# Kernel tuning notes

Hardware: AMD Instinct MI355X
Metric: run time of the kernel (lower is better)

Reference implementation:

```python
import math
import jax, jax.numpy as jnp
import numpy as np

N_HEADS, INPUT_DIM, EMBED_DIM = 8, 512, 512
KEY_DIM = EMBED_DIM // N_HEADS  # 64, val_dim == key_dim
BATCH, N = 4, 2048


def setup_inputs() -> dict:
    key = jax.random.key(0)
    ks = jax.random.split(key, 6)
    def unif(k, shape):
        stdv = 1.0 / math.sqrt(shape[-1])
        return jax.random.uniform(k, shape, jnp.float32, -stdv, stdv)
    q = jax.random.normal(ks[0], (BATCH, N, INPUT_DIM), jnp.float32)
    mask = jax.random.randint(ks[1], (BATCH, N, N), 0, 2, jnp.int32)
    W_query = unif(ks[2], (N_HEADS, INPUT_DIM, KEY_DIM))
    W_key = unif(ks[3], (N_HEADS, INPUT_DIM, KEY_DIM))
    W_val = unif(ks[4], (N_HEADS, INPUT_DIM, KEY_DIM))
    W_out = unif(ks[5], (N_HEADS, KEY_DIM, EMBED_DIM))
    return {"q": q, "mask": mask, "W_query": W_query, "W_key": W_key,
            "W_val": W_val, "W_out": W_out}


def reference(q, mask, W_query, W_key, W_val, W_out):
    # Self-attention: k is None, v is None -> k = q, v = q (module forward_).
    norm = 1.0 / math.sqrt(KEY_DIM)
    m = mask.astype(bool)[None]  # (1, b, nq, ng) broadcast over heads
    Q = jnp.einsum('bnd,hdk->hbnk', q, W_query)  # (h, b, nq, dk)
    K = jnp.einsum('bnd,hdk->hbnk', q, W_key)    # (h, b, ng, dk)
    V = jnp.einsum('bnd,hdv->hbnv', q, W_val)    # (h, b, ng, dv)
    scores = norm * jnp.einsum('hbqk,hbgk->hbqg', Q, K)  # (h, b, nq, ng)
    scores = jnp.where(m, -jnp.inf, scores)
    attn = jax.nn.softmax(scores, axis=-1)
    attn = jnp.where(m, 0.0, attn)  # zero out masked (also kills NaN rows)
    heads = jnp.einsum('hbqg,hbgv->hbqv', attn, V)
    out = jnp.einsum('hbqv,hve->bqe', heads, W_out)  # (b, nq, embed)
    return out
```

## Files before the change

kernel.cpp:

```cpp
#include <hip/hip_runtime.h>
#include <hip/hip_bf16.h>
#include <stdint.h>

using bf16 = __hip_bfloat16;
typedef __attribute__((ext_vector_type(8))) short short8;
typedef __attribute__((ext_vector_type(4))) short short4b;
typedef __attribute__((ext_vector_type(4))) float f32x4;
typedef __attribute__((ext_vector_type(4))) unsigned int u32x4;

#if __has_builtin(__builtin_amdgcn_exp2f)
#define EXP2(x) __builtin_amdgcn_exp2f(x)
#else
#define EXP2(x) exp2f(x)
#endif

__device__ __forceinline__ short8 load8(const bf16* p) {
  return *reinterpret_cast<const short8*>(p);
}
__device__ __forceinline__ short f2b(float f) {
  return __builtin_bit_cast(short, __float2bfloat16(f));
}
__device__ __forceinline__ unsigned int pk2(float a, float b) {
  return (unsigned int)(unsigned short)f2b(a) |
         ((unsigned int)(unsigned short)f2b(b) << 16);
}
__device__ __forceinline__ void asy16(const bf16* g, bf16* l) {
  __builtin_amdgcn_global_load_lds(
      (const __attribute__((address_space(1))) void*)g,
      (__attribute__((address_space(3))) void*)l, 16, 0, 0);
}


__global__ void k_prep(const float4* __restrict__ x, ushort4* __restrict__ xb,
                       const float* __restrict__ Wq, const float* __restrict__ Wk,
                       const float* __restrict__ Wv, const float* __restrict__ Wo,
                       bf16* __restrict__ Wcat, bf16* __restrict__ Wot,
                       const int4* __restrict__ m4,
                       unsigned long long* __restrict__ bits) {
  int blk = blockIdx.x;
  const int tid = threadIdx.x;
  if (blk < 4096) {
    int i = blk * 256 + tid;
    float4 v = x[i];
    ushort4 o;
    o.x = (unsigned short)f2b(v.x);
    o.y = (unsigned short)f2b(v.y);
    o.z = (unsigned short)f2b(v.z);
    o.w = (unsigned short)f2b(v.w);
    xb[i] = o;
  } else if (blk < 4352) {
    int t = blk - 4096;
    __shared__ float T[64][65];
    if (t < 192) {
      int which = t >> 6;
      int h = (t >> 3) & 7, dt = t & 7;
      const float* W = (which == 0) ? Wq : ((which == 1) ? Wk : Wv);
#pragma unroll
      for (int p = 0; p < 4; ++p) {
        int row = p * 16 + (tid >> 4);
        float4 v = *(const float4*)(W + (size_t)(h * 512 + dt * 64 + row) * 64 +
                                    (tid & 15) * 4);
        T[row][(tid & 15) * 4 + 0] = v.x;
        T[row][(tid & 15) * 4 + 1] = v.y;
        T[row][(tid & 15) * 4 + 2] = v.z;
        T[row][(tid & 15) * 4 + 3] = v.w;
      }
      __syncthreads();
      float scale = (which == 0) ? 0.18033688011112042f : 1.0f;
      int jj = tid >> 2, i0 = (tid & 3) * 16;
#pragma unroll
      for (int q = 0; q < 2; ++q) {
        short8 o;
#pragma unroll
        for (int e = 0; e < 8; ++e) o[e] = f2b(T[i0 + q * 8 + e][jj] * scale);
        *(short8*)(Wcat + (size_t)(which * 512 + h * 64 + jj) * 512 + dt * 64 +
                   i0 + q * 8) = o;
      }
    } else {
      int t2 = t - 192;
      int h = t2 >> 3, et = t2 & 7;
#pragma unroll
      for (int p = 0; p < 4; ++p) {
        int row = p * 16 + (tid >> 4);
        float4 v = *(const float4*)(Wo + (size_t)(h * 64 + row) * 512 + et * 64 +
                                    (tid & 15) * 4);
        T[row][(tid & 15) * 4 + 0] = v.x;
        T[row][(tid & 15) * 4 + 1] = v.y;
        T[row][(tid & 15) * 4 + 2] = v.z;
        T[row][(tid & 15) * 4 + 3] = v.w;
      }
      __syncthreads();
      int jj = tid >> 2, i0 = (tid & 3) * 16;
#pragma unroll
      for (int q = 0; q < 2; ++q) {
        short8 o;
#pragma unroll
        for (int e = 0; e < 8; ++e) o[e] = f2b(T[i0 + q * 8 + e][jj]);
        *(short8*)(Wot + (size_t)(et * 64 + jj) * 512 + h * 64 + i0 + q * 8) = o;
      }
    }
  } else {
    int i = (blk - 4352) * 256 + tid;
    int4 v = m4[i];
    unsigned int nib = (unsigned)(v.x != 0) | ((unsigned)(v.y != 0) << 1) |
                       ((unsigned)(v.z != 0) << 2) | ((unsigned)(v.w != 0) << 3);
    unsigned long long w = (unsigned long long)nib << (4 * (tid & 15));
    w |= __shfl_xor(w, 1);
    w |= __shfl_xor(w, 2);
    w |= __shfl_xor(w, 4);
    w |= __shfl_xor(w, 8);
    if ((tid & 15) == 0) bits[i >> 4] = w;
  }
}

__device__ __forceinline__ void gemm128(const bf16* __restrict__ A,
                                        const bf16* __restrict__ Bt,
                                        bf16* As, bf16* Bs,
                                        int rowBase, int colBase,
                                        f32x4 acc[4][4]) {
  const int tid = threadIdx.x;
  const int lane = tid & 63, w = tid >> 6;
  const int g = lane >> 4, r = lane & 15;

  auto stage = [&](int buf, int s) {
#pragma unroll
    for (int p = 0; p < 2; ++p) {
      int c = p * 256 + tid;
      int row = c >> 2, gr = c & 3, sg = gr ^ (row & 3);
      asy16(A + (size_t)(rowBase + row) * 512 + s * 32 + sg * 8,
            As + buf * 4096 + c * 8);
    }
#pragma unroll
    for (int p = 0; p < 2; ++p) {
      int c = p * 256 + tid;
      int row = c >> 2, gr = c & 3, sg = gr ^ (row & 3);
      asy16(Bt + (size_t)(colBase + row) * 512 + s * 32 + sg * 8,
            Bs + buf * 4096 + c * 8);
    }
  };

  stage(0, 0);
  int buf = 0;
  const int rbl = (w >> 1) * 64, cbl = (w & 1) * 64;
  for (int s = 0; s < 16; ++s) {
    __syncthreads();
    if (s < 15) stage(buf ^ 1, s + 1);
    const bf16* a0 = As + buf * 4096;
    const bf16* b0 = Bs + buf * 4096;
    short8 af[4], bfr[4];
#pragma unroll
    for (int mt = 0; mt < 4; ++mt) {
      int row = rbl + mt * 16 + r;
      af[mt] = load8(a0 + (row * 4 + (g ^ (row & 3))) * 8);
    }
#pragma unroll
    for (int nt = 0; nt < 4; ++nt) {
      int col = cbl + nt * 16 + r;
      bfr[nt] = load8(b0 + (col * 4 + (g ^ (col & 3))) * 8);
    }
#pragma unroll
    for (int mt = 0; mt < 4; ++mt)
#pragma unroll
      for (int nt = 0; nt < 4; ++nt)
        acc[mt][nt] = __builtin_amdgcn_mfma_f32_16x16x32_bf16(
            af[mt], bfr[nt], acc[mt][nt], 0, 0, 0);
    buf ^= 1;
  }
}

__global__ __launch_bounds__(256, 3) void k_proj_qkv(
    const bf16* __restrict__ Xb, const bf16* __restrict__ Wcat,
    bf16* __restrict__ Qb, bf16* __restrict__ Kp, bf16* __restrict__ Vp) {
  __shared__ __align__(16) bf16 As[2 * 4096];
  __shared__ __align__(16) bf16 Bs[2 * 4096];
  int rowBase = blockIdx.x * 128, colBase = blockIdx.y * 128;
  f32x4 acc[4][4] = {};
  gemm128(Xb, Wcat, As, Bs, rowBase, colBase, acc);
  const int lane = threadIdx.x & 63, w = threadIdx.x >> 6;
  const int g = lane >> 4, r = lane & 15;
#pragma unroll
  for (int mt = 0; mt < 4; ++mt) {
    int row0 = rowBase + (w >> 1) * 64 + mt * 16 + 4 * g;
    int b = row0 >> 11, n0 = row0 & 2047;
    int kt = n0 >> 6;
#pragma unroll
    for (int nt = 0; nt < 4; ++nt) {
      int col = colBase + (w & 1) * 64 + nt * 16 + r;
      if (col < 512) {
        int hh = col >> 6, dk = col & 63;
        bf16* p0 = Qb + ((size_t)(b * 8 + hh) * 2048 + n0) * 64 + dk;
#pragma unroll
        for (int rr = 0; rr < 4; ++rr)
          p0[rr * 64] = __float2bfloat16(acc[mt][nt][rr]);
      } else if (col < 1024) {
        int hh = (col >> 6) & 7, dk = col & 63;
        int half = dk >> 5, gk = (dk >> 3) & 3, jj = dk & 7;
        int kr = n0 & 63;
        int kc = kr >> 4, r0 = kr & 15;
        bf16* base = Kp + (size_t)(b * 8 + hh) * 131072 + (size_t)kt * 4096 +
                     ((kc * 2 + half) * 4 + gk) * 128 + jj;
#pragma unroll
        for (int rr = 0; rr < 4; ++rr)
          base[(r0 + rr) * 8] = __float2bfloat16(acc[mt][nt][rr]);
      } else {
        int hdv = col - 1024;
        int hh = hdv >> 6, dv = hdv & 63;
        int dvs = dv >> 4, rv = dv & 15;
        int kcol0 = n0 & 63;
        int half = kcol0 >> 5, gv = (kcol0 >> 2) & 3;
        int j0 = ((kcol0 >> 4) & 1) * 4;
        short4b pkv;
#pragma unroll
        for (int rr = 0; rr < 4; ++rr) pkv[rr] = f2b(acc[mt][nt][rr]);
        *reinterpret_cast<short4b*>(
            Vp + (size_t)(b * 8 + hh) * 131072 + (size_t)kt * 4096 +
            (((half * 4 + dvs) * 4 + gv) * 16 + rv) * 8 + j0) = pkv;
      }
    }
  }
}

__global__ __launch_bounds__(256, 2) void k_proj_out(
    const bf16* __restrict__ O, const bf16* __restrict__ Wot,
    float* __restrict__ out) {
  __shared__ __align__(16) bf16 As[2 * 4096];
  __shared__ __align__(16) bf16 Bs[2 * 4096];
  int rowBase = blockIdx.x * 128, colBase = blockIdx.y * 128;
  f32x4 acc[4][4] = {};
  gemm128(O, Wot, As, Bs, rowBase, colBase, acc);
  const int lane = threadIdx.x & 63, w = threadIdx.x >> 6;
  const int g = lane >> 4, r = lane & 15;
#pragma unroll
  for (int mt = 0; mt < 4; ++mt) {
    int row0 = rowBase + (w >> 1) * 64 + mt * 16 + 4 * g;
#pragma unroll
    for (int nt = 0; nt < 4; ++nt) {
      int col = colBase + (w & 1) * 64 + nt * 16 + r;
#pragma unroll
      for (int rr = 0; rr < 4; ++rr)
        out[(size_t)(row0 + rr) * 512 + col] = acc[mt][nt][rr];
    }
  }
}

__global__ __launch_bounds__(256, 4) void k_attn(const bf16* __restrict__ Q,
    const bf16* __restrict__ K, const bf16* __restrict__ V,
    const unsigned long long* __restrict__ MB, bf16* __restrict__ O) {
  const int blin = blockIdx.x;
  const int j = blin >> 3;
  const int bh = (blin & 7) * 4 + (j >> 5);
  const int qt = j & 31;
  const int b = bh >> 3, h = bh & 7;
  const int tid = threadIdx.x;
  const int lane = tid & 63;
  const int wave = tid >> 6;
  const int g = lane >> 4, r = lane & 15;
  const int qbase = qt * 64 + wave * 16;

  __shared__ __align__(16) bf16 Kl[2][4096];
  __shared__ __align__(16) bf16 Vl[2][4096];

  const bf16* Kp = K + (size_t)bh * 131072;
  const bf16* Vp = V + (size_t)bh * 131072;

  short8 qf0, qf1;
  {
    const bf16* Qp = Q + ((size_t)bh * 2048 + qbase + r) * 64;
    qf0 = load8(Qp + g * 8);
    qf1 = load8(Qp + 32 + g * 8);
  }
  const unsigned long long* Mp = MB + ((size_t)b * 2048 + qbase + r) * 32;

  short8 ones;
#pragma unroll
  for (int i = 0; i < 8; ++i) ones[i] = (short)0x3F80;

  f32x4 acc[4] = {};
  f32x4 acc_l = {};

  auto stageK = [&](int buf, int kt) {
    const bf16* Kg = Kp + (size_t)kt * 4096;
    asy16(Kg + tid * 8, &Kl[buf][0] + tid * 8);
    asy16(Kg + 2048 + tid * 8, &Kl[buf][0] + 2048 + tid * 8);
  };
  auto stageV = [&](int buf, int kt) {
    const bf16* Vg = Vp + (size_t)kt * 4096;
    asy16(Vg + tid * 8, &Vl[buf][0] + tid * 8);
    asy16(Vg + 2048 + tid * 8, &Vl[buf][0] + 2048 + tid * 8);
  };

  auto qk = [&](const bf16* kl, f32x4 stl[4]) {
#pragma unroll
    for (int kc = 0; kc < 4; ++kc) {
      short8 kf0 = load8(kl + ((kc * 2 + 0) * 4 + g) * 128 + r * 8);
      short8 kf1 = load8(kl + ((kc * 2 + 1) * 4 + g) * 128 + r * 8);
      f32x4 z = {};
      z = __builtin_amdgcn_mfma_f32_16x16x32_bf16(kf0, qf0, z, 0, 0, 0);
      stl[kc] = __builtin_amdgcn_mfma_f32_16x16x32_bf16(kf1, qf1, z, 0, 0, 0);
    }
  };

  stageK(0, 0);
  stageK(1, 1);
  stageV(0, 0);
  unsigned long long mw0, mw1;
  mw0 = Mp[0];
  __syncthreads();
  f32x4 st0[4], st1[4];
  qk(&Kl[0][0], st0);

#define ATTN_ITER(KT, CUR, NXT, SC, SN, MC, MN)                              \
  do {                                                                       \
    __syncthreads();                                                         \
    if ((KT) < 30) stageK(CUR, (KT) + 2);                                    \
    if ((KT) < 31) {                                                         \
      stageV(NXT, (KT) + 1);                                                 \
      MN = Mp[(KT) + 1];                                                     \
    }                                                                        \
    __builtin_amdgcn_s_setprio(1);                                           \
    if ((KT) < 31) qk(&Kl[NXT][0], SN);                                      \
    __builtin_amdgcn_s_setprio(0);                                           \
    unsigned ml = (unsigned)MC >> (4 * g);                                   \
    unsigned mh = (unsigned)(MC >> 32) >> (4 * g);                           \
    float p[16];                                                             \
    _Pragma("unroll") for (int kc = 0; kc < 4; ++kc)                         \
        _Pragma("unroll") for (int rr = 0; rr < 4; ++rr) {                   \
      float e = EXP2(SC[kc][rr]);                                            \
      unsigned wsel = (kc & 2) ? mh : ml;                                    \
      bool bad = (wsel >> (((kc & 1) << 4) + rr)) & 1u;                      \
      p[kc * 4 + rr] = bad ? 0.f : e;                                        \
    }                                                                        \
    u32x4 q0, q1;                                                            \
    _Pragma("unroll") for (int i2 = 0; i2 < 4; ++i2) {                       \
      q0[i2] = pk2(p[2 * i2], p[2 * i2 + 1]);                                \
      q1[i2] = pk2(p[8 + 2 * i2], p[8 + 2 * i2 + 1]);                        \
    }                                                                        \
    short8 pa0 = __builtin_bit_cast(short8, q0);                             \
    short8 pa1 = __builtin_bit_cast(short8, q1);                             \
    acc_l = __builtin_amdgcn_mfma_f32_16x16x32_bf16(pa0, ones, acc_l, 0, 0, 0); \
    acc_l = __builtin_amdgcn_mfma_f32_16x16x32_bf16(pa1, ones, acc_l, 0, 0, 0); \
    const bf16* vl = &Vl[CUR][0];                                            \
    __builtin_amdgcn_s_setprio(1);                                           \
    _Pragma("unroll") for (int dvs = 0; dvs < 4; ++dvs) {                    \
      short8 vb0 = load8(vl + ((0 * 4 + dvs) * 4 + g) * 128 + r * 8);        \
      short8 vb1 = load8(vl + ((1 * 4 + dvs) * 4 + g) * 128 + r * 8);        \
      acc[dvs] = __builtin_amdgcn_mfma_f32_16x16x32_bf16(pa0, vb0, acc[dvs], 0, 0, 0); \
      acc[dvs] = __builtin_amdgcn_mfma_f32_16x16x32_bf16(pa1, vb1, acc[dvs], 0, 0, 0); \
    }                                                                        \
    __builtin_amdgcn_s_setprio(0);                                           \
  } while (0)

  for (int t = 0; t < 16; ++t) {
    const int kt = 2 * t;
    ATTN_ITER(kt, 0, 1, st0, st1, mw0, mw1);
    ATTN_ITER(kt + 1, 1, 0, st1, st0, mw1, mw0);
  }
#undef ATTN_ITER

  float inv[4];
#pragma unroll
  for (int rr = 0; rr < 4; ++rr)
    inv[rr] = (acc_l[rr] > 0.f) ? 1.f / acc_l[rr] : 0.f;
  bf16* Op = O + ((size_t)b * 2048 + qbase + 4 * g) * 512 + h * 64;
#pragma unroll
  for (int dvs = 0; dvs < 4; ++dvs)
#pragma unroll
    for (int rr = 0; rr < 4; ++rr)
      Op[rr * 512 + dvs * 16 + r] = __float2bfloat16(acc[dvs][rr] * inv[rr]);
}


extern "C" void kernel_launch(void* const* d_in, const int* in_sizes, int n_in,
                              void* d_out, int out_size, void* d_ws, size_t ws_size,
                              hipStream_t stream) {
  const float* q    = (const float*)d_in[0];
  const int*   mask = (const int*)d_in[1];
  const float* Wq   = (const float*)d_in[2];
  const float* Wk   = (const float*)d_in[3];
  const float* Wv   = (const float*)d_in[4];
  const float* Wo   = (const float*)d_in[5];
  float* out = (float*)d_out;

  char* ws = (char*)d_ws;
  const size_t MB1 = 1024 * 1024;
  bf16* Xb   = (bf16*)(ws + 0);
  bf16* Qb   = (bf16*)(ws + 8 * MB1);
  bf16* Kpm  = (bf16*)(ws + 16 * MB1);
  bf16* Vpm  = (bf16*)(ws + 24 * MB1);
  bf16* Ob   = (bf16*)(ws + 32 * MB1);
  unsigned long long* Mbits = (unsigned long long*)(ws + 40 * MB1);
  bf16* Wcat = (bf16*)(ws + 42 * MB1);
  bf16* Wot  = (bf16*)(ws + 42 * MB1 + 1536 * 512 * 2);

  k_prep<<<20736, 256, 0, stream>>>((const float4*)q, (ushort4*)Xb,
                                    Wq, Wk, Wv, Wo, Wcat, Wot,
                                    (const int4*)mask, Mbits);
  k_proj_qkv<<<dim3(64, 12), 256, 0, stream>>>(Xb, Wcat, Qb, Kpm, Vpm);
  k_attn<<<1024, 256, 0, stream>>>(Qb, Kpm, Vpm, Mbits, Ob);
  k_proj_out<<<dim3(64, 4), 256, 0, stream>>>(Ob, Wot, out);
}
```

Before: 207.2 us.

## Double attention block size with triple-buffered K/V and smaller out-proj tiles

The attention kernel now runs 512-thread blocks covering 128 queries, so each staged K/V tile is shared by twice as many waves. K and V staging moves to a three-buffer ring, loaded together two tiles ahead, with one asynchronous copy per thread per tile. The output projection switches to 64x128 tiles with a new GEMM helper, doubling its block count to fill the GPU better. The O buffer now aliases the Xb workspace region, which relies on Xb no longer being needed after the QKV projection; the larger blocks and bigger shared-memory footprint may lower attention occupancy.

Measured after the change: 205.2 us. No clear change (-1.0%).

```diff
diff --git a/kernel.cpp b/kernel.cpp
--- a/kernel.cpp
+++ b/kernel.cpp
@@ -168,6 +168,60 @@
   }
 }
 
+__device__ __forceinline__ void gemm64x128(const bf16* __restrict__ A,
+                                           const bf16* __restrict__ Bt,
+                                           bf16* As, bf16* Bs,
+                                           int rowBase, int colBase,
+                                           f32x4 acc[2][4]) {
+  const int tid = threadIdx.x;
+  const int lane = tid & 63, w = tid >> 6;
+  const int g = lane >> 4, r = lane & 15;
+
+  auto stage = [&](int buf, int s) {
+    {
+      int c = tid;
+      int row = c >> 2, gr = c & 3, sg = gr ^ (row & 3);
+      asy16(A + (size_t)(rowBase + row) * 512 + s * 32 + sg * 8,
+            As + buf * 2048 + c * 8);
+    }
+#pragma unroll
+    for (int p = 0; p < 2; ++p) {
+      int c = p * 256 + tid;
+      int row = c >> 2, gr = c & 3, sg = gr ^ (row & 3);
+      asy16(Bt + (size_t)(colBase + row) * 512 + s * 32 + sg * 8,
+            Bs + buf * 4096 + c * 8);
+    }
+  };
+
+  stage(0, 0);
+  int buf = 0;
+  const int rbl = (w >> 1) * 32, cbl = (w & 1) * 64;
+  for (int s = 0; s < 16; ++s) {
+    __syncthreads();
+    if (s < 15) stage(buf ^ 1, s + 1);
+    const bf16* a0 = As + buf * 2048;
+    const bf16* b0 = Bs + buf * 4096;
+    short8 af[2], bfr[4];
+#pragma unroll
+    for (int mt = 0; mt < 2; ++mt) {
+      int row = rbl + mt * 16 + r;
+      af[mt] = load8(a0 + (row * 4 + (g ^ (row & 3))) * 8);
+    }
+#pragma unroll
+    for (int nt = 0; nt < 4; ++nt) {
+      int col = cbl + nt * 16 + r;
+      bfr[nt] = load8(b0 + (col * 4 + (g ^ (col & 3))) * 8);
+    }
+#pragma unroll
+    for (int mt = 0; mt < 2; ++mt)
+#pragma unroll
+      for (int nt = 0; nt < 4; ++nt)
+        acc[mt][nt] = __builtin_amdgcn_mfma_f32_16x16x32_bf16(
+            af[mt], bfr[nt], acc[mt][nt], 0, 0, 0);
+    buf ^= 1;
+  }
+}
+
 __global__ __launch_bounds__(256, 3) void k_proj_qkv(
     const bf16* __restrict__ Xb, const bf16* __restrict__ Wcat,
     bf16* __restrict__ Qb, bf16* __restrict__ Kp, bf16* __restrict__ Vp) {
@@ -220,19 +274,19 @@
   }
 }
 
-__global__ __launch_bounds__(256, 2) void k_proj_out(
+__global__ __launch_bounds__(256, 4) void k_proj_out(
     const bf16* __restrict__ O, const bf16* __restrict__ Wot,
     float* __restrict__ out) {
-  __shared__ __align__(16) bf16 As[2 * 4096];
+  __shared__ __align__(16) bf16 As[2 * 2048];
   __shared__ __align__(16) bf16 Bs[2 * 4096];
-  int rowBase = blockIdx.x * 128, colBase = blockIdx.y * 128;
-  f32x4 acc[4][4] = {};
-  gemm128(O, Wot, As, Bs, rowBase, colBase, acc);
+  int rowBase = blockIdx.x * 64, colBase = blockIdx.y * 128;
+  f32x4 acc[2][4] = {};
+  gemm64x128(O, Wot, As, Bs, rowBase, colBase, acc);
   const int lane = threadIdx.x & 63, w = threadIdx.x >> 6;
   const int g = lane >> 4, r = lane & 15;
 #pragma unroll
-  for (int mt = 0; mt < 4; ++mt) {
-    int row0 = rowBase + (w >> 1) * 64 + mt * 16 + 4 * g;
+  for (int mt = 0; mt < 2; ++mt) {
+    int row0 = rowBase + (w >> 1) * 32 + mt * 16 + 4 * g;
 #pragma unroll
     for (int nt = 0; nt < 4; ++nt) {
       int col = colBase + (w & 1) * 64 + nt * 16 + r;
@@ -243,22 +297,22 @@
   }
 }
 
-__global__ __launch_bounds__(256, 4) void k_attn(const bf16* __restrict__ Q,
+__global__ __launch_bounds__(512, 4) void k_attn(const bf16* __restrict__ Q,
     const bf16* __restrict__ K, const bf16* __restrict__ V,
     const unsigned long long* __restrict__ MB, bf16* __restrict__ O) {
   const int blin = blockIdx.x;
   const int j = blin >> 3;
-  const int bh = (blin & 7) * 4 + (j >> 5);
-  const int qt = j & 31;
+  const int bh = (blin & 7) * 4 + (j >> 4);
+  const int qt = j & 15;
   const int b = bh >> 3, h = bh & 7;
   const int tid = threadIdx.x;
   const int lane = tid & 63;
   const int wave = tid >> 6;
   const int g = lane >> 4, r = lane & 15;
-  const int qbase = qt * 64 + wave * 16;
-
-  __shared__ __align__(16) bf16 Kl[2][4096];
-  __shared__ __align__(16) bf16 Vl[2][4096];
+  const int qbase = qt * 128 + wave * 16;
+
+  __shared__ __align__(16) bf16 Kl[3][4096];
+  __shared__ __align__(16) bf16 Vl[3][4096];
 
   const bf16* Kp = K + (size_t)bh * 131072;
   const bf16* Vp = V + (size_t)bh * 131072;
@@ -278,15 +332,11 @@
   f32x4 acc[4] = {};
   f32x4 acc_l = {};
 
-  auto stageK = [&](int buf, int kt) {
+  auto stage = [&](int buf, int kt) {
     const bf16* Kg = Kp + (size_t)kt * 4096;
+    const bf16* Vg = Vp + (size_t)kt * 4096;
     asy16(Kg + tid * 8, &Kl[buf][0] + tid * 8);
-    asy16(Kg + 2048 + tid * 8, &Kl[buf][0] + 2048 + tid * 8);
-  };
-  auto stageV = [&](int buf, int kt) {
-    const bf16* Vg = Vp + (size_t)kt * 4096;
     asy16(Vg + tid * 8, &Vl[buf][0] + tid * 8);
-    asy16(Vg + 2048 + tid * 8, &Vl[buf][0] + 2048 + tid * 8);
   };
 
   auto qk = [&](const bf16* kl, f32x4 stl[4]) {
@@ -300,25 +350,21 @@
     }
   };
 
-  stageK(0, 0);
-  stageK(1, 1);
-  stageV(0, 0);
+  stage(0, 0);
+  stage(1, 1);
   unsigned long long mw0, mw1;
   mw0 = Mp[0];
   __syncthreads();
   f32x4 st0[4], st1[4];
   qk(&Kl[0][0], st0);
 
-#define ATTN_ITER(KT, CUR, NXT, SC, SN, MC, MN)                              \
+#define ATTN_ITER(KT, CUR, NXT, STG, SC, SN, MC, MN, DO_STAGE, DO_NEXT)      \
   do {                                                                       \
     __syncthreads();                                                         \
-    if ((KT) < 30) stageK(CUR, (KT) + 2);                                    \
-    if ((KT) < 31) {                                                         \
-      stageV(NXT, (KT) + 1);                                                 \
-      MN = Mp[(KT) + 1];                                                     \
-    }                                                                        \
+    if (DO_STAGE) stage(STG, (KT) + 2);                                      \
+    if (DO_NEXT) MN = Mp[(KT) + 1];                                          \
     __builtin_amdgcn_s_setprio(1);                                           \
-    if ((KT) < 31) qk(&Kl[NXT][0], SN);                                      \
+    if (DO_NEXT) qk(&Kl[NXT][0], SN);                                        \
     __builtin_amdgcn_s_setprio(0);                                           \
     unsigned ml = (unsigned)MC >> (4 * g);                                   \
     unsigned mh = (unsigned)(MC >> 32) >> (4 * g);                           \
@@ -350,11 +396,17 @@
     __builtin_amdgcn_s_setprio(0);                                           \
   } while (0)
 
-  for (int t = 0; t < 16; ++t) {
-    const int kt = 2 * t;
-    ATTN_ITER(kt, 0, 1, st0, st1, mw0, mw1);
-    ATTN_ITER(kt + 1, 1, 0, st1, st0, mw1, mw0);
-  }
+  for (int t = 0; t < 5; ++t) {
+    const int kt = 6 * t;
+    ATTN_ITER(kt + 0, 0, 1, 2, st0, st1, mw0, mw1, true, true);
+    ATTN_ITER(kt + 1, 1, 2, 0, st1, st0, mw1, mw0, true, true);
+    ATTN_ITER(kt + 2, 2, 0, 1, st0, st1, mw0, mw1, true, true);
+    ATTN_ITER(kt + 3, 0, 1, 2, st1, st0, mw1, mw0, true, true);
+    ATTN_ITER(kt + 4, 1, 2, 0, st0, st1, mw0, mw1, true, true);
+    ATTN_ITER(kt + 5, 2, 0, 1, st1, st0, mw1, mw0, true, true);
+  }
+  ATTN_ITER(30, 0, 1, 2, st0, st1, mw0, mw1, false, true);
+  ATTN_ITER(31, 1, 2, 0, st1, st0, mw1, mw0, false, false);
 #undef ATTN_ITER
 
   float inv[4];
@@ -384,18 +436,18 @@
   char* ws = (char*)d_ws;
   const size_t MB1 = 1024 * 1024;
   bf16* Xb   = (bf16*)(ws + 0);
+  bf16* Ob   = (bf16*)(ws + 0);
   bf16* Qb   = (bf16*)(ws + 8 * MB1);
   bf16* Kpm  = (bf16*)(ws + 16 * MB1);
   bf16* Vpm  = (bf16*)(ws + 24 * MB1);
-  bf16* Ob   = (bf16*)(ws + 32 * MB1);
-  unsigned long long* Mbits = (unsigned long long*)(ws + 40 * MB1);
-  bf16* Wcat = (bf16*)(ws + 42 * MB1);
-  bf16* Wot  = (bf16*)(ws + 42 * MB1 + 1536 * 512 * 2);
+  unsigned long long* Mbits = (unsigned long long*)(ws + 32 * MB1);
+  bf16* Wcat = (bf16*)(ws + 34 * MB1);
+  bf16* Wot  = (bf16*)(ws + 34 * MB1 + 1536 * 512 * 2);
 
   k_prep<<<20736, 256, 0, stream>>>((const float4*)q, (ushort4*)Xb,
                                     Wq, Wk, Wv, Wo, Wcat, Wot,
                                     (const int4*)mask, Mbits);
   k_proj_qkv<<<dim3(64, 12), 256, 0, stream>>>(Xb, Wcat, Qb, Kpm, Vpm);
-  k_attn<<<1024, 256, 0, stream>>>(Qb, Kpm, Vpm, Mbits, Ob);
-  k_proj_out<<<dim3(64, 4), 256, 0, stream>>>(Ob, Wot, out);
-}
+  k_attn<<<512, 512, 0, stream>>>(Qb, Kpm, Vpm, Mbits, Ob);
+  k_proj_out<<<dim3(128, 4), 256, 0, stream>>>(Ob, Wot, out);
+}
```
